# Kernel tuning notes

Hardware: AMD Instinct MI355X
Metric: run time of the kernel (lower is better)

Reference implementation:

```python
import jax, jax.numpy as jnp
import numpy as np
from jax import lax

VOCAB = 100000
INPUT_DIM = 100
HIDDEN_DIM = 10
OUTPUT_DIM = 1
BATCH = 1024
SEQ = 512


def setup_inputs() -> dict:
    key = jax.random.key(0)
    ks = jax.random.split(key, 8)
    bound_ih = 1.0 / np.sqrt(HIDDEN_DIM)
    inp = {
        "x": jax.random.randint(ks[0], (BATCH, SEQ), 0, VOCAB, dtype=jnp.int32),
        "emb": jax.random.normal(ks[1], (VOCAB, INPUT_DIM), dtype=jnp.float32),
        "W_ih": jax.random.uniform(ks[2], (HIDDEN_DIM, INPUT_DIM), jnp.float32, -bound_ih, bound_ih),
        "b_ih": jax.random.uniform(ks[3], (HIDDEN_DIM,), jnp.float32, -bound_ih, bound_ih),
        "W_hh": jax.random.uniform(ks[4], (HIDDEN_DIM, HIDDEN_DIM), jnp.float32, -bound_ih, bound_ih),
        "b_hh": jax.random.uniform(ks[5], (HIDDEN_DIM,), jnp.float32, -bound_ih, bound_ih),
        "W_fc": jax.random.uniform(ks[6], (OUTPUT_DIM, HIDDEN_DIM), jnp.float32, -bound_ih, bound_ih),
        "b_fc": jax.random.uniform(ks[7], (OUTPUT_DIM,), jnp.float32, -bound_ih, bound_ih),
    }
    return inp


def reference(x, emb, W_ih, b_ih, W_hh, b_hh, W_fc, b_fc):
    # Embedding lookup: [B, S, INPUT_DIM]
    xe = emb[x]
    # Precompute input projection for all timesteps in one GEMM: [B, S, H]
    pre = jnp.einsum("bsd,hd->bsh", xe, W_ih) + b_ih

    def step(h, p_t):
        # h: [B, H], p_t: [B, H]
        h_new = jax.nn.relu(p_t + h @ W_hh.T + b_hh)
        return h_new, None

    h0 = jnp.zeros((x.shape[0], W_hh.shape[0]), dtype=pre.dtype)
    hn, _ = lax.scan(step, h0, jnp.swapaxes(pre, 0, 1))  # scan over time
    # torch returns hn of shape [layer_dim=1, B, H]; fc + sigmoid on hn
    out = jax.nn.sigmoid(hn @ W_fc.T + b_fc)[None, :, :]  # [1, B, 1]
    return out
```

## Files before the change

### kernel.cpp

```cpp
#include <hip/hip_runtime.h>
#include <hip/hip_bf16.h>
#include <math.h>

#define VOCAB 100000
#define INPUT_DIM 100
#define HIDDEN_DIM 10
#define BATCH 1024
#define SEQ 512

__global__ __launch_bounds__(128) void proj_kernel(
    const float* __restrict__ emb, const float* __restrict__ W_ih,
    const float* __restrict__ b_ih, const float* __restrict__ b_hh,
    float* __restrict__ proj) {
  int v = blockIdx.x * blockDim.x + threadIdx.x;
  if (v >= VOCAB) return;

  const float4* e4 = (const float4*)(emb + (size_t)v * INPUT_DIM);
  const float4* W4 = (const float4*)W_ih;

  float4 e[25];
#pragma unroll
  for (int d = 0; d < 25; ++d) e[d] = e4[d];

  float acc[HIDDEN_DIM];
#pragma unroll
  for (int i = 0; i < HIDDEN_DIM; ++i) acc[i] = b_ih[i] + b_hh[i];

#pragma unroll
  for (int d = 0; d < 25; ++d) {
#pragma unroll
    for (int i = 0; i < HIDDEN_DIM; ++i) {
      float4 w = W4[i * 25 + d];
      acc[i] = fmaf(e[d].x, w.x, acc[i]);
      acc[i] = fmaf(e[d].y, w.y, acc[i]);
      acc[i] = fmaf(e[d].z, w.z, acc[i]);
      acc[i] = fmaf(e[d].w, w.w, acc[i]);
    }
  }

  float2* p2 = (float2*)(proj + (size_t)v * HIDDEN_DIM);
#pragma unroll
  for (int i = 0; i < 5; ++i) p2[i] = make_float2(acc[2 * i], acc[2 * i + 1]);
}

__global__ __launch_bounds__(256, 1) void scan_kernel(
    const int* __restrict__ x, const float* __restrict__ proj,
    const float* __restrict__ W_hh, const float* __restrict__ W_fc,
    const float* __restrict__ b_fc, float* __restrict__ out) {
  __shared__ int sIdx[4][SEQ];

  int lane = threadIdx.x & 63;
  int widx = threadIdx.x >> 6;
  int b = __builtin_amdgcn_readfirstlane((int)(blockIdx.x * 4 + widx));
  int i = (lane < HIDDEN_DIM) ? lane : 0;

  float Wr[HIDDEN_DIM];
#pragma unroll
  for (int j = 0; j < HIDDEN_DIM; ++j) Wr[j] = W_hh[i * HIDDEN_DIM + j];
  float wfc = (lane < HIDDEN_DIM) ? W_fc[lane] : 0.f;

  const int4* xb4 = (const int4*)(x + (size_t)b * SEQ);
  int4* s4 = (int4*)(sIdx[widx]);
  s4[lane] = xb4[lane];
  s4[64 + lane] = xb4[64 + lane];

  const float* projLane = proj + i;
  float h = 0.f;

#define LOADIDX(Q0, Q1, base)                              \
  {                                                        \
    int bc_ = (base) <= (SEQ - 8) ? (base) : (SEQ - 8);    \
    Q0 = s4[bc_ >> 2];                                     \
    Q1 = s4[(bc_ >> 2) + 1];                               \
  }
#define GATHER(P, Q0, Q1)                                  \
  P[0] = projLane[(unsigned)Q0.x * 10u];                   \
  P[1] = projLane[(unsigned)Q0.y * 10u];                   \
  P[2] = projLane[(unsigned)Q0.z * 10u];                   \
  P[3] = projLane[(unsigned)Q0.w * 10u];                   \
  P[4] = projLane[(unsigned)Q1.x * 10u];                   \
  P[5] = projLane[(unsigned)Q1.y * 10u];                   \
  P[6] = projLane[(unsigned)Q1.z * 10u];                   \
  P[7] = projLane[(unsigned)Q1.w * 10u];
#define COMPUTE(P)                                         \
  _Pragma("unroll") for (int u = 0; u < 8; ++u) {          \
    float hj[HIDDEN_DIM];                                  \
    _Pragma("unroll") for (int j = 0; j < HIDDEN_DIM; ++j) \
      hj[j] = __uint_as_float(                             \
          __builtin_amdgcn_readlane(__float_as_uint(h), j)); \
    float a0 = fmaf(Wr[0], hj[0], P[u]);                   \
    float a1 = Wr[1] * hj[1];                              \
    a0 = fmaf(Wr[2], hj[2], a0);                           \
    a1 = fmaf(Wr[3], hj[3], a1);                           \
    a0 = fmaf(Wr[4], hj[4], a0);                           \
    a1 = fmaf(Wr[5], hj[5], a1);                           \
    a0 = fmaf(Wr[6], hj[6], a0);                           \
    a1 = fmaf(Wr[7], hj[7], a1);                           \
    a0 = fmaf(Wr[8], hj[8], a0);                           \
    a1 = fmaf(Wr[9], hj[9], a1);                           \
    h = fmaxf(a0 + a1, 0.f);                               \
  }

  int4 Ia0, Ia1, Ib0, Ib1, Ic0, Ic1, Id0, Id1;
  float pA[8], pB[8], pC[8], pD[8];

  LOADIDX(Ia0, Ia1, 0) LOADIDX(Ib0, Ib1, 8) LOADIDX(Ic0, Ic1, 16)
  GATHER(pA, Ia0, Ia1) GATHER(pB, Ib0, Ib1) GATHER(pC, Ic0, Ic1)
  LOADIDX(Id0, Id1, 24)

  for (int tt = 0; tt < SEQ; tt += 32) {
    GATHER(pD, Id0, Id1) LOADIDX(Ia0, Ia1, tt + 32) COMPUTE(pA)
    GATHER(pA, Ia0, Ia1) LOADIDX(Ib0, Ib1, tt + 40) COMPUTE(pB)
    GATHER(pB, Ib0, Ib1) LOADIDX(Ic0, Ic1, tt + 48) COMPUTE(pC)
    GATHER(pC, Ic0, Ic1) LOADIDX(Id0, Id1, tt + 56) COMPUTE(pD)
  }
#undef LOADIDX
#undef GATHER
#undef COMPUTE

  float prod = wfc * h;
  float z = 0.f;
#pragma unroll
  for (int j = 0; j < HIDDEN_DIM; ++j)
    z += __uint_as_float(__builtin_amdgcn_readlane(__float_as_uint(prod), j));
  if (lane == 0) out[b] = 1.f / (1.f + expf(-(z + b_fc[0])));
}

extern "C" void kernel_launch(void* const* d_in, const int* in_sizes, int n_in,
                              void* d_out, int out_size, void* d_ws, size_t ws_size,
                              hipStream_t stream) {
  const int*   x    = (const int*)d_in[0];
  const float* emb  = (const float*)d_in[1];
  const float* W_ih = (const float*)d_in[2];
  const float* b_ih = (const float*)d_in[3];
  const float* W_hh = (const float*)d_in[4];
  const float* b_hh = (const float*)d_in[5];
  const float* W_fc = (const float*)d_in[6];
  const float* b_fc = (const float*)d_in[7];
  float* out = (float*)d_out;

  float* proj = (float*)d_ws;

  int blocksA = (VOCAB + 127) / 128;
  proj_kernel<<<blocksA, 128, 0, stream>>>(emb, W_ih, b_ih, b_hh, proj);

  int blocksB = BATCH / 4;
  scan_kernel<<<blocksB, 256, 0, stream>>>(x, proj, W_hh, W_fc, b_fc, out);
}
```

Baseline: 132.8 us.

## Stage embedding rows in LDS with coalesced loads and split hidden outputs across threads

The projection kernel now loads a 64-row tile of the embedding table with fully coalesced scalar loads into padded shared memory, instead of having each thread read its own 400-byte row with strided float4 loads. Each row's ten outputs are then split across four threads, so every thread computes two or three dot products from LDS. This targets the uncoalesced global access and high register pressure of the old per-row scheme. In exchange it adds a block barrier, LDS traffic and scalar stores to proj.

```diff
diff --git a/kernel.cpp b/kernel.cpp
--- a/kernel.cpp
+++ b/kernel.cpp
@@ -8,39 +8,57 @@
 #define BATCH 1024
 #define SEQ 512
 
-__global__ __launch_bounds__(128) void proj_kernel(
+#define ROWS_PER_BLK 64
+#define LDS_PITCH 101
+
+__global__ __launch_bounds__(256) void proj_kernel(
     const float* __restrict__ emb, const float* __restrict__ W_ih,
     const float* __restrict__ b_ih, const float* __restrict__ b_hh,
     float* __restrict__ proj) {
-  int v = blockIdx.x * blockDim.x + threadIdx.x;
-  if (v >= VOCAB) return;
+  __shared__ float se[ROWS_PER_BLK * LDS_PITCH];
 
-  const float4* e4 = (const float4*)(emb + (size_t)v * INPUT_DIM);
-  const float4* W4 = (const float4*)W_ih;
-
-  float4 e[25];
-#pragma unroll
-  for (int d = 0; d < 25; ++d) e[d] = e4[d];
-
-  float acc[HIDDEN_DIM];
-#pragma unroll
-  for (int i = 0; i < HIDDEN_DIM; ++i) acc[i] = b_ih[i] + b_hh[i];
+  const int t = threadIdx.x;
+  const size_t base = (size_t)blockIdx.x * (ROWS_PER_BLK * INPUT_DIM);
+  const size_t TOT = (size_t)VOCAB * INPUT_DIM;
 
 #pragma unroll
-  for (int d = 0; d < 25; ++d) {
+  for (int l = 0; l < 25; ++l) {
+    int n = t + 256 * l;
+    size_t g = base + n;
+    float val = (g < TOT) ? emb[g] : 0.f;
+    int r = n / 100;
+    int k = n - r * 100;
+    se[r * LDS_PITCH + k] = val;
+  }
+  __syncthreads();
+
+  const int row = t & 63;
+  const int q = t >> 6;
+  const int v = blockIdx.x * ROWS_PER_BLK + row;
+
+  const float* W0 = W_ih + q * INPUT_DIM;
+  const float* W1 = W_ih + (q + 4) * INPUT_DIM;
+  const float* W2 = W_ih + ((q < 2) ? (q + 8) : q) * INPUT_DIM;
+
+  float acc0 = b_ih[q] + b_hh[q];
+  float acc1 = b_ih[q + 4] + b_hh[q + 4];
+  float acc2 = (q < 2) ? (b_ih[q + 8] + b_hh[q + 8]) : 0.f;
+
+  const float* er = se + row * LDS_PITCH;
 #pragma unroll
-    for (int i = 0; i < HIDDEN_DIM; ++i) {
-      float4 w = W4[i * 25 + d];
-      acc[i] = fmaf(e[d].x, w.x, acc[i]);
-      acc[i] = fmaf(e[d].y, w.y, acc[i]);
-      acc[i] = fmaf(e[d].z, w.z, acc[i]);
-      acc[i] = fmaf(e[d].w, w.w, acc[i]);
-    }
+  for (int k = 0; k < INPUT_DIM; ++k) {
+    float e = er[k];
+    acc0 = fmaf(e, W0[k], acc0);
+    acc1 = fmaf(e, W1[k], acc1);
+    acc2 = fmaf(e, W2[k], acc2);
   }
 
-  float2* p2 = (float2*)(proj + (size_t)v * HIDDEN_DIM);
-#pragma unroll
-  for (int i = 0; i < 5; ++i) p2[i] = make_float2(acc[2 * i], acc[2 * i + 1]);
+  if (v < VOCAB) {
+    float* pv = proj + (size_t)v * HIDDEN_DIM;
+    pv[q] = acc0;
+    pv[q + 4] = acc1;
+    if (q < 2) pv[q + 8] = acc2;
+  }
 }
 
 __global__ __launch_bounds__(256, 1) void scan_kernel(
@@ -141,8 +159,8 @@
 
   float* proj = (float*)d_ws;
 
-  int blocksA = (VOCAB + 127) / 128;
-  proj_kernel<<<blocksA, 128, 0, stream>>>(emb, W_ih, b_ih, b_hh, proj);
+  int blocksA = (VOCAB + ROWS_PER_BLK - 1) / ROWS_PER_BLK;
+  proj_kernel<<<blocksA, 256, 0, stream>>>(emb, W_ih, b_ih, b_hh, proj);
 
   int blocksB = BATCH / 4;
   scan_kernel<<<blocksB, 256, 0, stream>>>(x, proj, W_hh, W_fc, b_fc, out);
```

Measured after the change: 149.2 us. +12.3%, slower.
